# Kernel tuning notes

Hardware: AMD Instinct MI355X
Metric: run time of the kernel (lower is better)

## Reference

```python
import jax, jax.numpy as jnp
import numpy as np

EPS = 1e-8
SCALE_FACTOR = 5.0
ITERS = 3

def _ln(x, g, b):
    m = x.mean(-1, keepdims=True)
    v = ((x - m) ** 2).mean(-1, keepdims=True)
    return (x - m) / jnp.sqrt(v + 1e-5) * g + b

def setup_inputs() -> dict:
    key = jax.random.key(0)
    ks = jax.random.split(key, 12)
    B, N, K, D = 8, 1024, 8, 256
    n01 = lambda k, s, sc=0.02: jax.random.normal(k, s, jnp.float32) * sc
    return {
        "inputs": jax.random.normal(ks[0], (B, N, D), jnp.float32),
        "conditioning": jax.random.normal(ks[1], (B, K, D + 4), jnp.float32),
        "ni_g": jnp.ones((D,), jnp.float32), "ni_b": jnp.zeros((D,), jnp.float32),
        "ns_g": jnp.ones((D,), jnp.float32), "ns_b": jnp.zeros((D,), jnp.float32),
        "wq": n01(ks[2], (D, D)), "wk": n01(ks[3], (D, D)), "wv": n01(ks[4], (D, D)),
        "gp_w": n01(ks[5], (2, D), 0.5), "gp_b": jnp.zeros((D,), jnp.float32),
        "ge_ln_g": jnp.ones((D,), jnp.float32), "ge_ln_b": jnp.zeros((D,), jnp.float32),
        "ge_w1": n01(ks[6], (D, 2 * D)), "ge_b1": jnp.zeros((2 * D,), jnp.float32),
        "ge_w2": n01(ks[7], (2 * D, D)), "ge_b2": jnp.zeros((D,), jnp.float32),
        "gru_wih": n01(ks[8], (3 * D, D)), "gru_whh": n01(ks[9], (3 * D, D)),
        "gru_bih": jnp.zeros((3 * D,), jnp.float32), "gru_bhh": jnp.zeros((3 * D,), jnp.float32),
    }

def _forward(inputs, conditioning, ni_g, ni_b, ns_g, ns_b, wq, wk, wv,
             gp_w, gp_b, ge_ln_g, ge_ln_b, ge_w1, ge_b1, ge_w2, ge_b2,
             gru_wih, gru_whh, gru_bih, gru_bhh):
    B, N, FD = inputs.shape
    D = wq.shape[1]
    attn_scale = D ** -0.5
    side = int(round(N ** 0.5))
    xs = jnp.linspace(-1.0, 1.0, side)
    abs_grid = jnp.stack(jnp.meshgrid(xs, xs, indexing="ij"), -1).reshape(N, 2)  # (N,2)

    x = _ln(inputs, ni_g, ni_b)
    k = x @ wk  # (B,N,D)
    v = x @ wv  # (B,N,D)

    def grid_enc(t):
        h = _ln(t, ge_ln_g, ge_ln_b)
        h = jax.nn.relu(h @ ge_w1 + ge_b1)
        return h @ ge_w2 + ge_b2

    def step(slots_full, update):
        slots = slots_full[..., :-4]                       # (B,K,D)
        pos = jnp.clip(slots_full[..., -4:-2], -1.0, 1.0)  # (B,K,2)
        scl = jnp.clip(slots_full[..., -2:], 1e-3, 2.0)    # (B,K,2)
        rel_grid = (abs_grid[None, None] - pos[:, :, None]) / (scl[:, :, None] * SCALE_FACTOR)  # (B,K,N,2)
        rel_enc = rel_grid @ gp_w + gp_b                   # (B,K,N,D)
        rel_k = grid_enc(k[:, None] + rel_enc)             # (B,K,N,D)
        rel_v = grid_enc(v[:, None] + rel_enc)             # (B,K,N,D)
        q = _ln(slots, ns_g, ns_b) @ wq                    # (B,K,D)
        dots = jnp.einsum("bkd,bknd->bkn", q, rel_k) * attn_scale
        attn0 = jax.nn.softmax(dots, axis=1)               # softmax over the SLOT axis
        attn = attn0 + EPS
        attn = attn / attn.sum(-1, keepdims=True)
        pos_n = jnp.einsum("bkn,nd->bkd", attn0, abs_grid)
        spread = (abs_grid[None, None] - pos_n[:, :, None]) ** 2  # (B,K,N,2)
        scl_n = jnp.clip(jnp.sqrt(jnp.einsum("bkn,bknd->bkd", attn0 + EPS, spread)), 1e-3, 2.0)
        if update:
            upd = jnp.einsum("bknd,bkn->bkd", rel_v, attn)
            gx = upd @ gru_wih.T + gru_bih
            gh = slots @ gru_whh.T + gru_bhh
            xr, xz, xn = jnp.split(gx, 3, -1)
            hr, hz, hn = jnp.split(gh, 3, -1)
            r = jax.nn.sigmoid(xr + hr)
            z = jax.nn.sigmoid(xz + hz)
            n_ = jnp.tanh(xn + r * hn)
            slots = (1.0 - z) * n_ + z * slots
        return jnp.concatenate([slots, pos_n, scl_n], -1), attn0, rel_grid

    attn0 = rel_grid = None
    for i in range(ITERS + 1):
        conditioning, attn0, rel_grid = step(conditioning, i < ITERS)
    return conditioning, attn0, rel_grid

def reference(inputs, conditioning, ni_g, ni_b, ns_g, ns_b, wq, wk, wv,
              gp_w, gp_b, ge_ln_g, ge_ln_b, ge_w1, ge_b1, ge_w2, ge_b2,
              gru_wih, gru_whh, gru_bih, gru_bhh):
    return _forward(inputs, conditioning, ni_g, ni_b, ns_g, ns_b, wq, wk, wv,
                    gp_w, gp_b, ge_ln_g, ge_ln_b, ge_w1, ge_b1, ge_w2, ge_b2,
                    gru_wih, gru_whh, gru_bih, gru_bhh)
```

## Files before the change

kernel.cpp:

```cpp
#include <hip/hip_runtime.h>
#include <math.h>

#define NB 8
#define NN 1024
#define NK 8
#define ND 256
#define ND2 512
#define NBK 64
#define EPSA 1e-8f
#define LNEPS 1e-5f
#define GSTEP (2.0f/31.0f)

using short8 = __attribute__((ext_vector_type(8))) short;
using short4v = __attribute__((ext_vector_type(4))) short;
using floatx4 = __attribute__((ext_vector_type(4))) float;

__device__ __forceinline__ short f2bf(float f) {
  unsigned u = __builtin_bit_cast(unsigned, f);
  u += 0x7fffu + ((u >> 16) & 1u);
  return (short)(u >> 16);
}
__device__ __forceinline__ float bf2f(short s) {
  unsigned u = ((unsigned)(unsigned short)s) << 16;
  return __builtin_bit_cast(float, u);
}

__global__ __launch_bounds__(256) void k_cvt_all(
    const float* __restrict__ w1, const float* __restrict__ w2,
    const float* __restrict__ wk, const float* __restrict__ wv,
    const float* __restrict__ wih, const float* __restrict__ whh,
    const float* __restrict__ wq, const float* __restrict__ b2,
    short* __restrict__ w1T, short* __restrict__ wkT, short* __restrict__ wvT,
    short* __restrict__ whhB, short* __restrict__ w2B,
    float* __restrict__ bx, float* __restrict__ vb) {
  const int idx = blockIdx.x * 256 + threadIdx.x;
  if (idx < 131072) {
    const int n = idx >> 8, k = idx & 255;
    const int dst = ((n >> 4) * 8 + (k >> 5)) * 512 + ((k >> 3) & 3) * 128 + (n & 15) * 8 + (k & 7);
    w1T[dst] = f2bf(w1[(size_t)k * 512 + n]);
  } else if (idx < 196608) {
    const int i = idx - 131072;
    const int n = i >> 8, k = i & 255;
    const int dst = ((n >> 4) * 8 + (k >> 5)) * 512 + ((k >> 3) & 3) * 128 + (n & 15) * 8 + (k & 7);
    wkT[dst] = f2bf(wk[(size_t)k * 256 + n]);
  } else if (idx < 262144) {
    const int i = idx - 196608;
    const int n = i >> 8, k = i & 255;
    const int dst = ((n >> 4) * 8 + (k >> 5)) * 512 + ((k >> 3) & 3) * 128 + (n & 15) * 8 + (k & 7);
    wvT[dst] = f2bf(wv[(size_t)k * 256 + n]);
  } else if (idx < 458752) {
    const int i = idx - 262144;
    whhB[i] = f2bf(whh[i]);
  } else if (idx < 589824) {
    const int i = idx - 458752;
    w2B[i] = f2bf(w2[i]);
  } else if (idx < 590592) {
    const int j = idx - 589824;
    float s = 0.f;
#pragma unroll 8
    for (int d = 0; d < 256; d++) s = fmaf(b2[d], wih[(size_t)j * 256 + d], s);
    bx[j] = s;
  } else if (idx < 590848) {
    const int e = idx - 590592;
    float s = 0.f;
#pragma unroll 8
    for (int d = 0; d < 256; d++) s = fmaf(wq[(size_t)e * 256 + d], b2[d], s);
    vb[e] = s;
  }
}

__global__ __launch_bounds__(256, 2) void k_mm(
    const float* __restrict__ wih, const float* __restrict__ wq,
    const short* __restrict__ w2B,
    short* __restrict__ WXT, short* __restrict__ MQ) {
  const int z = blockIdx.z;
  if (z == 1 && blockIdx.x >= 4) return;
  const float* __restrict__ A = z ? wq : wih;
  short* __restrict__ C = z ? MQ : WXT;
  __shared__ __align__(16) short As[64 * 264];
  const int row0 = blockIdx.x * 64;
  const int col0 = blockIdx.y * 128;
  const int t = threadIdx.x;
  const int wave = t >> 6, lane = t & 63, l15 = lane & 15, quad = lane >> 4;
  {
    const int r = t >> 2, sub = t & 3;
    const float* ar = A + (size_t)(row0 + r) * 256;
#pragma unroll
    for (int ii = 0; ii < 16; ii++) {
      const int d = sub * 4 + ii * 16;
      const float4 v = *(const float4*)(ar + d);
      short4v pk = {f2bf(v.x), f2bf(v.y), f2bf(v.z), f2bf(v.w)};
      *(short4v*)&As[r * 264 + d] = pk;
    }
  }
  __syncthreads();
  const short* wp = w2B + (size_t)(col0 + wave * 32 + l15) * 256 + quad * 8;
  floatx4 acc[4][2];
#pragma unroll
  for (int mt = 0; mt < 4; mt++)
#pragma unroll
    for (int nt = 0; nt < 2; nt++) acc[mt][nt] = (floatx4){0.f, 0.f, 0.f, 0.f};
#pragma unroll
  for (int kk = 0; kk < 8; kk++) {
    short8 af[4];
#pragma unroll
    for (int mt = 0; mt < 4; mt++)
      af[mt] = *(const short8*)&As[(mt * 16 + l15) * 264 + kk * 32 + quad * 8];
    short8 bf[2];
#pragma unroll
    for (int nt = 0; nt < 2; nt++)
      bf[nt] = *(const short8*)(wp + nt * 16 * 256 + kk * 32);
#pragma unroll
    for (int mt = 0; mt < 4; mt++)
#pragma unroll
      for (int nt = 0; nt < 2; nt++)
        acc[mt][nt] = __builtin_amdgcn_mfma_f32_16x16x32_bf16(af[mt], bf[nt], acc[mt][nt], 0, 0, 0);
  }
#pragma unroll
  for (int mt = 0; mt < 4; mt++)
#pragma unroll
    for (int nt = 0; nt < 2; nt++)
#pragma unroll
      for (int j = 0; j < 4; j++)
        C[(size_t)(row0 + mt * 16 + quad * 4 + j) * 512 + col0 + wave * 32 + nt * 16 + l15] =
            f2bf(acc[mt][nt][j]);
}

__global__ __launch_bounds__(256, 2) void k_gemm_kv_mfma(
    const float* __restrict__ inp,
    const float* __restrict__ nig, const float* __restrict__ nib,
    const short* __restrict__ wkT, const short* __restrict__ wvT,
    float* __restrict__ kout, float* __restrict__ vout) {
  __shared__ __align__(16) short tln[64 * 264];
  const short* __restrict__ WT = blockIdx.z ? wvT : wkT;
  float* __restrict__ out = blockIdx.z ? vout : kout;
  const int row0 = blockIdx.x * 64;
  const int t = threadIdx.x;
  const int wave = t >> 6, lane = t & 63, l15 = lane & 15, quad = lane >> 4;
  {
    const int r = t >> 2, sub = t & 3;
    const float* xr = inp + (size_t)(row0 + r) * ND;
    float tv[64];
    float sum = 0.f, ssq = 0.f;
#pragma unroll
    for (int ii = 0; ii < 16; ii++) {
      const int d = sub * 4 + ii * 16;
      const float4 xv = *(const float4*)(xr + d);
      tv[ii * 4 + 0] = xv.x; sum += xv.x; ssq += xv.x * xv.x;
      tv[ii * 4 + 1] = xv.y; sum += xv.y; ssq += xv.y * xv.y;
      tv[ii * 4 + 2] = xv.z; sum += xv.z; ssq += xv.z * xv.z;
      tv[ii * 4 + 3] = xv.w; sum += xv.w; ssq += xv.w * xv.w;
    }
    sum += __shfl_xor(sum, 1); ssq += __shfl_xor(ssq, 1);
    sum += __shfl_xor(sum, 2); ssq += __shfl_xor(ssq, 2);
    const float mean = sum * (1.0f / ND);
    const float var = ssq * (1.0f / ND) - mean * mean;
    const float rstd = rsqrtf(var + LNEPS);
#pragma unroll
    for (int ii = 0; ii < 16; ii++) {
      const int d = sub * 4 + ii * 16;
      const float4 gg = *(const float4*)(nig + d);
      const float4 bb = *(const float4*)(nib + d);
      short4v pk;
      pk.x = f2bf((tv[ii * 4 + 0] - mean) * rstd * gg.x + bb.x);
      pk.y = f2bf((tv[ii * 4 + 1] - mean) * rstd * gg.y + bb.y);
      pk.z = f2bf((tv[ii * 4 + 2] - mean) * rstd * gg.z + bb.z);
      pk.w = f2bf((tv[ii * 4 + 3] - mean) * rstd * gg.w + bb.w);
      *(short4v*)&tln[r * 264 + d] = pk;
    }
  }
  __syncthreads();
  floatx4 acc[4][4];
#pragma unroll
  for (int mt = 0; mt < 4; mt++)
#pragma unroll
    for (int nt = 0; nt < 4; nt++) acc[mt][nt] = (floatx4){0.f, 0.f, 0.f, 0.f};
  const short* wp = WT + (size_t)(wave * 32) * 512 + (size_t)lane * 8;
#pragma unroll
  for (int kk = 0; kk < 8; kk++) {
    short8 af[4];
#pragma unroll
    for (int mt = 0; mt < 4; mt++)
      af[mt] = *(const short8*)&tln[(mt * 16 + l15) * 264 + kk * 32 + quad * 8];
    short8 bf[4];
#pragma unroll
    for (int nt = 0; nt < 4; nt++)
      bf[nt] = *(const short8*)(wp + (nt * 8 + kk) * 512);
#pragma unroll
    for (int mt = 0; mt < 4; mt++)
#pragma unroll
      for (int nt = 0; nt < 4; nt++)
        acc[mt][nt] = __builtin_amdgcn_mfma_f32_16x16x32_bf16(af[mt], bf[nt], acc[mt][nt], 0, 0, 0);
  }
#pragma unroll
  for (int mt = 0; mt < 4; mt++)
#pragma unroll
    for (int nt = 0; nt < 4; nt++)
#pragma unroll
      for (int j = 0; j < 4; j++)
        out[(size_t)(row0 + mt * 16 + quad * 4 + j) * ND + wave * 64 + nt * 16 + l15] = acc[mt][nt][j];
}

#define LDA 264

__global__ __launch_bounds__(256, 2) void k_fused_mfma(
    const float* __restrict__ kv,
    const float* __restrict__ pos, const float* __restrict__ scl,
    const float* __restrict__ gpw, const float* __restrict__ gpb,
    const float* __restrict__ lng, const float* __restrict__ lnb,
    const short* __restrict__ w1T, const float* __restrict__ b1,
    const float* __restrict__ w2q, float* __restrict__ dots,
    const float* __restrict__ attn0, const float* __restrict__ stage,
    float* __restrict__ ph, const int mode) {
  __shared__ __align__(16) short tln[64 * LDA];

  const int bk = blockIdx.y;
  const int n0 = blockIdx.x * 64;
  const int b = bk >> 3;
  const int t = threadIdx.x;
  const int wave = t >> 6;
  const int lane = t & 63;
  const int l15 = lane & 15;
  const int quad = lane >> 4;

  {
    const float p0 = pos[bk * 2 + 0], p1 = pos[bk * 2 + 1];
    const float s0i = 1.0f / (scl[bk * 2 + 0] * 5.0f);
    const float s1i = 1.0f / (scl[bk * 2 + 1] * 5.0f);
    const int r = t >> 2;
    const int sub = t & 3;
    const int n = n0 + r;
    const float gx = -1.0f + GSTEP * (float)(n >> 5);
    const float gy = -1.0f + GSTEP * (float)(n & 31);
    const float rg0 = (gx - p0) * s0i;
    const float rg1 = (gy - p1) * s1i;
    const float* kvrow = kv + (size_t)(b * NN + n) * ND;
    float tv[64];
    float sum = 0.f, ssq = 0.f;
#pragma unroll
    for (int ii = 0; ii < 16; ii++) {
      const int d = sub * 4 + ii * 16;
      const float4 kv4 = *(const float4*)(kvrow + d);
      const float4 wa = *(const float4*)(gpw + d);
      const float4 wb = *(const float4*)(gpw + ND + d);
      const float4 pb = *(const float4*)(gpb + d);
      float v0 = kv4.x + rg0 * wa.x + rg1 * wb.x + pb.x;
      float v1 = kv4.y + rg0 * wa.y + rg1 * wb.y + pb.y;
      float v2 = kv4.z + rg0 * wa.z + rg1 * wb.z + pb.z;
      float v3 = kv4.w + rg0 * wa.w + rg1 * wb.w + pb.w;
      tv[ii * 4 + 0] = v0; sum += v0; ssq += v0 * v0;
      tv[ii * 4 + 1] = v1; sum += v1; ssq += v1 * v1;
      tv[ii * 4 + 2] = v2; sum += v2; ssq += v2 * v2;
      tv[ii * 4 + 3] = v3; sum += v3; ssq += v3 * v3;
    }
    sum += __shfl_xor(sum, 1); ssq += __shfl_xor(ssq, 1);
    sum += __shfl_xor(sum, 2); ssq += __shfl_xor(ssq, 2);
    const float mean = sum * (1.0f / ND);
    const float var = ssq * (1.0f / ND) - mean * mean;
    const float rstd = rsqrtf(var + LNEPS);
#pragma unroll
    for (int ii = 0; ii < 16; ii++) {
      const int d = sub * 4 + ii * 16;
      const float4 gg = *(const float4*)(lng + d);
      const float4 bb = *(const float4*)(lnb + d);
      short4v pk;
      pk.x = f2bf((tv[ii * 4 + 0] - mean) * rstd * gg.x + bb.x);
      pk.y = f2bf((tv[ii * 4 + 1] - mean) * rstd * gg.y + bb.y);
      pk.z = f2bf((tv[ii * 4 + 2] - mean) * rstd * gg.z + bb.z);
      pk.w = f2bf((tv[ii * 4 + 3] - mean) * rstd * gg.w + bb.w);
      *(short4v*)&tln[r * LDA + d] = pk;
    }
  }
  __syncthreads();

  floatx4 acc1[4][8];
#pragma unroll
  for (int mt = 0; mt < 4; mt++)
#pragma unroll
    for (int nt = 0; nt < 8; nt++) acc1[mt][nt] = (floatx4){0.f, 0.f, 0.f, 0.f};

  const short* w1p = w1T + (size_t)(wave * 64) * 512 + (size_t)lane * 8;
#pragma unroll
  for (int kk = 0; kk < 8; kk++) {
    short8 af[4];
#pragma unroll
    for (int mt = 0; mt < 4; mt++)
      af[mt] = *(const short8*)&tln[(mt * 16 + l15) * LDA + kk * 32 + quad * 8];
    short8 bf[8];
#pragma unroll
    for (int nt = 0; nt < 8; nt++)
      bf[nt] = *(const short8*)(w1p + (nt * 8 + kk) * 512);
#pragma unroll
    for (int mt = 0; mt < 4; mt++)
#pragma unroll
      for (int nt = 0; nt < 8; nt++)
        acc1[mt][nt] = __builtin_amdgcn_mfma_f32_16x16x32_bf16(af[mt], bf[nt], acc1[mt][nt], 0, 0, 0);
  }

  float b1v[8];
#pragma unroll
  for (int nt = 0; nt < 8; nt++) b1v[nt] = b1[wave * 128 + nt * 16 + l15];

  if (mode == 0) {
    float w2qv[8];
#pragma unroll
    for (int nt = 0; nt < 8; nt++) w2qv[nt] = w2q[bk * 512 + wave * 128 + nt * 16 + l15];
    const float qb2 = stage[bk * 8 + 5];
    __syncthreads();
    float* dred = (float*)tln;
#pragma unroll
    for (int mt = 0; mt < 4; mt++)
#pragma unroll
      for (int j = 0; j < 4; j++) {
        float p = 0.f;
#pragma unroll
        for (int nt = 0; nt < 8; nt++)
          p = fmaf(fmaxf(acc1[mt][nt][j] + b1v[nt], 0.f), w2qv[nt], p);
        p += __shfl_xor(p, 1); p += __shfl_xor(p, 2);
        p += __shfl_xor(p, 4); p += __shfl_xor(p, 8);
        if (l15 == 0) dred[wave * 64 + mt * 16 + quad * 4 + j] = p;
      }
    __syncthreads();
    if (t < 64) {
      const float s = dred[t] + dred[64 + t] + dred[128 + t] + dred[192 + t];
      dots[bk * NN + n0 + t] = (s + qb2) * 0.0625f;
    }
  } else {
    const float dn = 1.0f / (stage[bk * 8 + 0] + (float)NN * EPSA);
    float aw[4][4];
#pragma unroll
    for (int mt = 0; mt < 4; mt++)
#pragma unroll
      for (int j = 0; j < 4; j++)
        aw[mt][j] = (attn0[bk * NN + n0 + mt * 16 + quad * 4 + j] + EPSA) * dn;
#pragma unroll
    for (int nt = 0; nt < 8; nt++) {
      float cs = 0.f;
#pragma unroll
      for (int mt = 0; mt < 4; mt++)
#pragma unroll
        for (int j = 0; j < 4; j++)
          cs = fmaf(aw[mt][j], fmaxf(acc1[mt][nt][j] + b1v[nt], 0.f), cs);
      cs += __shfl_xor(cs, 16); cs += __shfl_xor(cs, 32);
      if (quad == 0) atomicAdd(ph + bk * 512 + wave * 128 + nt * 16 + l15, cs);
    }
  }
}

__global__ __launch_bounds__(256) void k_softmax_reduce(
    const float* __restrict__ dots, float* __restrict__ attn0,
    float* __restrict__ stage) {
  const int t = threadIdx.x;
  const int idx = blockIdx.x * 256 + t;
  const int b = idx >> 10, n = idx & 1023;
  const int lane = t & 63, wave = t >> 6;
  float vals[NK];
  float mx = -1e30f;
#pragma unroll
  for (int k = 0; k < NK; k++) {
    vals[k] = dots[(size_t)(b * NK + k) * NN + n];
    mx = fmaxf(mx, vals[k]);
  }
  float s = 0.f;
#pragma unroll
  for (int k = 0; k < NK; k++) { vals[k] = expf(vals[k] - mx); s += vals[k]; }
  const float inv = 1.0f / s;
  const float gx = -1.0f + GSTEP * (float)(n >> 5);
  const float gy = -1.0f + GSTEP * (float)(n & 31);
  const float gx2 = gx * gx, gy2 = gy * gy;
  float sk[NK][5];
#pragma unroll
  for (int k = 0; k < NK; k++) {
    const float a = vals[k] * inv;
    attn0[(size_t)(b * NK + k) * NN + n] = a;
    const float w = a + EPSA;
    sk[k][0] = a;
    sk[k][1] = a * gx;
    sk[k][2] = a * gy;
    sk[k][3] = w * gx2;
    sk[k][4] = w * gy2;
  }
#pragma unroll
  for (int m = 32; m >= 1; m >>= 1)
#pragma unroll
    for (int k = 0; k < NK; k++)
#pragma unroll
      for (int c = 0; c < 5; c++)
        sk[k][c] += __shfl_xor(sk[k][c], m);
  __shared__ float red[4][40];
  if (lane == 0) {
#pragma unroll
    for (int k = 0; k < NK; k++)
#pragma unroll
      for (int c = 0; c < 5; c++)
        red[wave][k * 5 + c] = sk[k][c];
  }
  __syncthreads();
  if (t < 40) {
    const float tot = red[0][t] + red[1][t] + red[2][t] + red[3][t];
    const int k = t / 5, c = t % 5;
    atomicAdd(&stage[(b * NK + k) * 8 + c], tot);
  }
}

__global__ __launch_bounds__(256) void k_gatesC(
    const float* __restrict__ ph, const float* __restrict__ sf,
    const short* __restrict__ WXT, const short* __restrict__ whhB,
    const float* __restrict__ bx, short* __restrict__ gxh) {
  __shared__ __align__(16) short A[64 * 264];
  const int c = blockIdx.x;
  const int isX = (c < 6) ? 1 : 0;
  const int jb = (isX ? c : c - 6) * 128;
  const int t = threadIdx.x;
  const int wave = t >> 6, lane = t & 63, l15 = lane & 15, quad = lane >> 4;
  const int r = t >> 2, sub = t & 3;
  floatx4 acc[4][2];
#pragma unroll
  for (int mt = 0; mt < 4; mt++)
#pragma unroll
    for (int nt = 0; nt < 2; nt++) acc[mt][nt] = (floatx4){0.f, 0.f, 0.f, 0.f};

  if (isX) {
#pragma unroll
    for (int half = 0; half < 2; half++) {
      if (half > 0) __syncthreads();
#pragma unroll
      for (int ii = 0; ii < 16; ii++) {
        const int d = sub * 4 + ii * 16;
        const float4 v = *(const float4*)(ph + r * 512 + half * 256 + d);
        short4v pk = {f2bf(v.x), f2bf(v.y), f2bf(v.z), f2bf(v.w)};
        *(short4v*)&A[r * 264 + d] = pk;
      }
      __syncthreads();
      const short* wp = WXT + (size_t)(jb + wave * 32 + l15) * 512 + half * 256 + quad * 8;
#pragma unroll
      for (int kk = 0; kk < 8; kk++) {
        short8 af[4];
#pragma unroll
        for (int mt = 0; mt < 4; mt++)
          af[mt] = *(const short8*)&A[(mt * 16 + l15) * 264 + kk * 32 + quad * 8];
        short8 bf[2];
#pragma unroll
        for (int nt = 0; nt < 2; nt++)
          bf[nt] = *(const short8*)(wp + nt * 16 * 512 + kk * 32);
#pragma unroll
        for (int mt = 0; mt < 4; mt++)
#pragma unroll
          for (int nt = 0; nt < 2; nt++)
            acc[mt][nt] = __builtin_amdgcn_mfma_f32_16x16x32_bf16(af[mt], bf[nt], acc[mt][nt], 0, 0, 0);
      }
    }
#pragma unroll
    for (int nt = 0; nt < 2; nt++) {
      const int col = jb + wave * 32 + nt * 16 + l15;
      const float bxv = bx[col];
#pragma unroll
      for (int mt = 0; mt < 4; mt++)
#pragma unroll
        for (int j = 0; j < 4; j++)
          gxh[(mt * 16 + quad * 4 + j) * 1536 + col] = f2bf(acc[mt][nt][j] + bxv);
    }
  } else {
#pragma unroll
    for (int ii = 0; ii < 16; ii++) {
      const int d = sub * 4 + ii * 16;
      const float4 v = *(const float4*)(sf + r * 260 + d);
      short4v pk = {f2bf(v.x), f2bf(v.y), f2bf(v.z), f2bf(v.w)};
      *(short4v*)&A[r * 264 + d] = pk;
    }
    __syncthreads();
    const short* wp = whhB + (size_t)(jb + wave * 32 + l15) * 256 + quad * 8;
#pragma unroll
    for (int kk = 0; kk < 8; kk++) {
      short8 af[4];
#pragma unroll
      for (int mt = 0; mt < 4; mt++)
        af[mt] = *(const short8*)&A[(mt * 16 + l15) * 264 + kk * 32 + quad * 8];
      short8 bf[2];
#pragma unroll
      for (int nt = 0; nt < 2; nt++)
        bf[nt] = *(const short8*)(wp + nt * 16 * 256 + kk * 32);
#pragma unroll
      for (int mt = 0; mt < 4; mt++)
#pragma unroll
        for (int nt = 0; nt < 2; nt++)
          acc[mt][nt] = __builtin_amdgcn_mfma_f32_16x16x32_bf16(af[mt], bf[nt], acc[mt][nt], 0, 0, 0);
    }
#pragma unroll
    for (int mt = 0; mt < 4; mt++)
#pragma unroll
      for (int nt = 0; nt < 2; nt++)
#pragma unroll
        for (int j = 0; j < 4; j++)
          gxh[(mt * 16 + quad * 4 + j) * 1536 + 768 + jb + wave * 32 + nt * 16 + l15] =
              f2bf(acc[mt][nt][j]);
    }
}

__global__ __launch_bounds__(256) void k_slotW(
    const short* __restrict__ gxh, float* __restrict__ sf,
    const float* __restrict__ cond,
    const float* __restrict__ bih, const float* __restrict__ bhh,
    const float* __restrict__ nsg, const float* __restrict__ nsb,
    const short* __restrict__ MQ, const float* __restrict__ vb,
    float* __restrict__ w2q, float* __restrict__ pos, float* __restrict__ scl,
    float* __restrict__ stage, float* __restrict__ ph, const int mode) {
  const int bk = blockIdx.x, t = threadIdx.x;
  __shared__ float lnvS[256];
  __shared__ float red[8];
  const int wv = t >> 6;
  float ns;
  if (mode) {
    const float h = sf[bk * 260 + t];
    const float x0 = bf2f(gxh[bk * 1536 + t]);
    const float x1 = bf2f(gxh[bk * 1536 + 256 + t]);
    const float x2 = bf2f(gxh[bk * 1536 + 512 + t]);
    const float h0 = bf2f(gxh[bk * 1536 + 768 + t]);
    const float h1v = bf2f(gxh[bk * 1536 + 1024 + t]);
    const float h2 = bf2f(gxh[bk * 1536 + 1280 + t]);
    const float r = 1.0f / (1.0f + expf(-(x0 + bih[t] + h0 + bhh[t])));
    const float z = 1.0f / (1.0f + expf(-(x1 + bih[256 + t] + h1v + bhh[256 + t])));
    const float nw = tanhf(x2 + bih[512 + t] + r * (h2 + bhh[512 + t]));
    ns = (1.0f - z) * nw + z * h;
    sf[bk * 260 + t] = ns;
  } else {
    ns = cond[bk * 260 + t];
    sf[bk * 260 + t] = ns;
    if (t < 4) sf[bk * 260 + 256 + t] = cond[bk * 260 + 256 + t];
  }
  float s2 = ns, ss = ns * ns;
#pragma unroll
  for (int m = 32; m >= 1; m >>= 1) { s2 += __shfl_xor(s2, m); ss += __shfl_xor(ss, m); }
  if ((t & 63) == 0) { red[wv] = s2; red[4 + wv] = ss; }
  __syncthreads();
  const float S = red[0] + red[1] + red[2] + red[3];
  const float SS = red[4] + red[5] + red[6] + red[7];
  const float mean = S * (1.0f / ND);
  const float var = SS * (1.0f / ND) - mean * mean;
  const float rstd = rsqrtf(var + LNEPS);
  const float lnv = (ns - mean) * rstd * nsg[t] + nsb[t];
  lnvS[t] = lnv;
  if (mode) {
    if (t == 0) {
      const float Sa = stage[bk * 8 + 0];
      const float G0 = stage[bk * 8 + 1];
      const float G1 = stage[bk * 8 + 2];
      const float Q0 = stage[bk * 8 + 3];
      const float Q1 = stage[bk * 8 + 4];
      const float W = Sa + (float)NN * EPSA;
      const float sc0 = sqrtf(fmaxf(Q0 - 2.0f * G0 * G0 + G0 * G0 * W, 0.f));
      const float sc1 = sqrtf(fmaxf(Q1 - 2.0f * G1 * G1 + G1 * G1 * W, 0.f));
      const float sc0c = fminf(fmaxf(sc0, 1e-3f), 2.0f);
      const float sc1c = fminf(fmaxf(sc1, 1e-3f), 2.0f);
      sf[bk * 260 + 256] = G0;
      sf[bk * 260 + 257] = G1;
      sf[bk * 260 + 258] = sc0c;
      sf[bk * 260 + 259] = sc1c;
      pos[bk * 2 + 0] = fminf(fmaxf(G0, -1.0f), 1.0f);
      pos[bk * 2 + 1] = fminf(fmaxf(G1, -1.0f), 1.0f);
      scl[bk * 2 + 0] = sc0c;
      scl[bk * 2 + 1] = sc1c;
    }
  } else {
    if (t < 2) {
      const float p = cond[bk * 260 + 256 + t];
      pos[bk * 2 + t] = fminf(fmaxf(p, -1.0f), 1.0f);
      const float sc = cond[bk * 260 + 258 + t];
      scl[bk * 2 + t] = fminf(fmaxf(sc, 1e-3f), 2.0f);
    }
  }
  __syncthreads();
  if (t < 5) stage[bk * 8 + t] = 0.f;
  ph[bk * 512 + t] = 0.f;
  ph[bk * 512 + 256 + t] = 0.f;
  float w0 = 0.f, w1v = 0.f;
#pragma unroll 8
  for (int e = 0; e < ND; e++) {
    const float lv = lnvS[e];
    w0 = fmaf(lv, bf2f(MQ[e * 512 + t]), w0);
    w1v = fmaf(lv, bf2f(MQ[e * 512 + 256 + t]), w1v);
  }
  w2q[bk * 512 + t] = w0;
  w2q[bk * 512 + 256 + t] = w1v;
  float qd = lnvS[t] * vb[t];
#pragma unroll
  for (int m = 32; m >= 1; m >>= 1) qd += __shfl_xor(qd, m);
  __syncthreads();
  if ((t & 63) == 0) red[wv] = qd;
  __syncthreads();
  if (t == 0) stage[bk * 8 + 5] = red[0] + red[1] + red[2] + red[3];
}

__global__ __launch_bounds__(256) void k_finalize(
    const float* __restrict__ sf, const float* __restrict__ attn0,
    const float* __restrict__ pos, const float* __restrict__ scl,
    const float* __restrict__ stage, float* __restrict__ out) {
  const int bk = blockIdx.x, t = threadIdx.x;
  out[bk * 260 + t] = sf[bk * 260 + t];
  if (t == 0) {
    const float Sa = stage[bk * 8 + 0];
    const float G0 = stage[bk * 8 + 1];
    const float G1 = stage[bk * 8 + 2];
    const float Q0 = stage[bk * 8 + 3];
    const float Q1 = stage[bk * 8 + 4];
    const float W = Sa + (float)NN * EPSA;
    const float sc0 = sqrtf(fmaxf(Q0 - 2.0f * G0 * G0 + G0 * G0 * W, 0.f));
    const float sc1 = sqrtf(fmaxf(Q1 - 2.0f * G1 * G1 + G1 * G1 * W, 0.f));
    out[bk * 260 + 256] = G0;
    out[bk * 260 + 257] = G1;
    out[bk * 260 + 258] = fminf(fmaxf(sc0, 1e-3f), 2.0f);
    out[bk * 260 + 259] = fminf(fmaxf(sc1, 1e-3f), 2.0f);
  }
  const float p0 = pos[bk * 2 + 0], p1 = pos[bk * 2 + 1];
  const float s0 = scl[bk * 2 + 0] * 5.0f, s1 = scl[bk * 2 + 1] * 5.0f;
#pragma unroll
  for (int i = 0; i < 4; i++) {
    const int n = t + 256 * i;
    out[16640 + bk * NN + n] = attn0[(size_t)bk * NN + n];
    const float gx = -1.0f + GSTEP * (float)(n >> 5);
    const float gy = -1.0f + GSTEP * (float)(n & 31);
    float2 v;
    v.x = (gx - p0) / s0;
    v.y = (gy - p1) / s1;
    *(float2*)(out + 16640 + 65536 + ((size_t)bk * NN + n) * 2) = v;
  }
}

extern "C" void kernel_launch(void* const* d_in, const int* in_sizes, int n_in,
                              void* d_out, int out_size, void* d_ws, size_t ws_size,
                              hipStream_t stream) {
  const float* inputs   = (const float*)d_in[0];
  const float* cond     = (const float*)d_in[1];
  const float* ni_g     = (const float*)d_in[2];
  const float* ni_b     = (const float*)d_in[3];
  const float* ns_g     = (const float*)d_in[4];
  const float* ns_b     = (const float*)d_in[5];
  const float* wq       = (const float*)d_in[6];
  const float* wk       = (const float*)d_in[7];
  const float* wv       = (const float*)d_in[8];
  const float* gp_w     = (const float*)d_in[9];
  const float* gp_b     = (const float*)d_in[10];
  const float* ge_ln_g  = (const float*)d_in[11];
  const float* ge_ln_b  = (const float*)d_in[12];
  const float* ge_w1    = (const float*)d_in[13];
  const float* ge_b1    = (const float*)d_in[14];
  const float* ge_w2    = (const float*)d_in[15];
  const float* ge_b2    = (const float*)d_in[16];
  const float* gru_wih  = (const float*)d_in[17];
  const float* gru_whh  = (const float*)d_in[18];
  const float* gru_bih  = (const float*)d_in[19];
  const float* gru_bhh  = (const float*)d_in[20];

  float* ws   = (float*)d_ws;
  float* kbuf = ws;
  float* vbuf = kbuf + 2097152;
  float* sf   = vbuf + 2097152;
  float* w2qb = sf + 16640;
  float* posb = w2qb + 32768;
  float* sclb = posb + 128;
  float* dotsb = sclb + 128;
  float* at0  = dotsb + 65536;
  float* phb  = at0 + 65536;
  float* stag = phb + 32768;
  float* bxb  = stag + 512;
  float* vbb  = bxb + 768;
  short* gxh  = (short*)(vbb + 256);
  short* w1T  = gxh + 98304;
  short* wkT  = w1T + 131072;
  short* wvT  = wkT + 65536;
  short* whhB = wvT + 65536;
  short* w2B  = whhB + 196608;
  short* WXT  = w2B + 131072;
  short* MQ   = WXT + 393216;

  float* out = (float*)d_out;

  k_cvt_all<<<2308, 256, 0, stream>>>(ge_w1, ge_w2, wk, wv, gru_wih, gru_whh, wq,
                                      ge_b2, w1T, wkT, wvT, whhB, w2B, bxb, vbb);
  k_mm<<<dim3(12, 4, 2), 256, 0, stream>>>(gru_wih, wq, w2B, WXT, MQ);
  k_gemm_kv_mfma<<<dim3(128, 1, 2), 256, 0, stream>>>(inputs, ni_g, ni_b,
                                                      wkT, wvT, kbuf, vbuf);
  k_slotW<<<NBK, 256, 0, stream>>>(gxh, sf, cond, gru_bih, gru_bhh, ns_g, ns_b,
                                   MQ, vbb, w2qb, posb, sclb, stag, phb, 0);

  for (int s = 0; s < 4; s++) {
    k_fused_mfma<<<dim3(16, NBK), 256, 0, stream>>>(
        kbuf, posb, sclb, gp_w, gp_b, ge_ln_g, ge_ln_b, w1T, ge_b1,
        w2qb, dotsb, at0, stag, phb, 0);
    k_softmax_reduce<<<32, 256, 0, stream>>>(dotsb, at0, stag);
    if (s < 3) {
      k_fused_mfma<<<dim3(16, NBK), 256, 0, stream>>>(
          vbuf, posb, sclb, gp_w, gp_b, ge_ln_g, ge_ln_b, w1T, ge_b1,
          w2qb, dotsb, at0, stag, phb, 1);
      k_gatesC<<<12, 256, 0, stream>>>(phb, sf, WXT, whhB, bxb, gxh);
      k_slotW<<<NBK, 256, 0, stream>>>(gxh, sf, cond, gru_bih, gru_bhh, ns_g, ns_b,
                                       MQ, vbb, w2qb, posb, sclb, stag, phb, 1);
    }
  }

  k_finalize<<<NBK, 256, 0, stream>>>(sf, at0, posb, sclb, stag, out);
}
```

Baseline: 447.3 us.

## Hoist slot-independent grid-encoder GEMM out of iterations via LayerNorm decomposition

The grid-encoder input is k (or v) plus a rank-2 positional term, so its LayerNorm moments and the first linear layer are expanded algebraically. The slot-independent part (x+gp_b)*g @ W1 is computed once per k and v with MFMA and stored as bf16. Each iteration then rebuilds the pre-activation from that, a few rank-1 correction vectors and per-row moments, removing the 64 GEMMs per slot per iteration. The attention-weighted reduction now writes per-block partials to a buffer that a separate kernel sums, replacing the atomics. The cost is a larger workspace, more memory traffic reading the bf16 KW rows for every slot, and numerics that now depend on the moment-based variance formula.

```diff
diff --git a/kernel.cpp b/kernel.cpp
--- a/kernel.cpp
+++ b/kernel.cpp
@@ -201,150 +201,284 @@
         out[(size_t)(row0 + mt * 16 + quad * 4 + j) * ND + wave * 64 + nt * 16 + l15] = acc[mt][nt][j];
 }
 
-#define LDA 264
-
-__global__ __launch_bounds__(256, 2) void k_fused_mfma(
-    const float* __restrict__ kv,
+__global__ __launch_bounds__(256, 2) void k_kw(
+    const float* __restrict__ kbuf, const float* __restrict__ vbuf,
+    const float* __restrict__ gpb, const float* __restrict__ gpw,
+    const float* __restrict__ lng,
+    const short* __restrict__ w1T,
+    short* __restrict__ KWk, short* __restrict__ KWv,
+    float* __restrict__ momk, float* __restrict__ momv) {
+  __shared__ __align__(16) short tln[64 * 264];
+  const float* __restrict__ src = blockIdx.z ? vbuf : kbuf;
+  short* __restrict__ KW = blockIdx.z ? KWv : KWk;
+  float* __restrict__ mom = blockIdx.z ? momv : momk;
+  const int row0 = blockIdx.x * 64;
+  const int t = threadIdx.x;
+  const int wave = t >> 6, lane = t & 63, l15 = lane & 15, quad = lane >> 4;
+  {
+    const int r = t >> 2, sub = t & 3;
+    const float* xr = src + (size_t)(row0 + r) * ND;
+    float su = 0.f, sq = 0.f, sa = 0.f, sb = 0.f;
+#pragma unroll
+    for (int ii = 0; ii < 16; ii++) {
+      const int d = sub * 4 + ii * 16;
+      const float4 xv = *(const float4*)(xr + d);
+      const float4 pb = *(const float4*)(gpb + d);
+      const float4 wa = *(const float4*)(gpw + d);
+      const float4 wb = *(const float4*)(gpw + ND + d);
+      const float4 gg = *(const float4*)(lng + d);
+      const float u0 = xv.x + pb.x, u1 = xv.y + pb.y, u2 = xv.z + pb.z, u3 = xv.w + pb.w;
+      su += u0 + u1 + u2 + u3;
+      sq += u0 * u0 + u1 * u1 + u2 * u2 + u3 * u3;
+      sa += u0 * wa.x + u1 * wa.y + u2 * wa.z + u3 * wa.w;
+      sb += u0 * wb.x + u1 * wb.y + u2 * wb.z + u3 * wb.w;
+      short4v pk = {f2bf(u0 * gg.x), f2bf(u1 * gg.y), f2bf(u2 * gg.z), f2bf(u3 * gg.w)};
+      *(short4v*)&tln[r * 264 + d] = pk;
+    }
+    su += __shfl_xor(su, 1); sq += __shfl_xor(sq, 1);
+    sa += __shfl_xor(sa, 1); sb += __shfl_xor(sb, 1);
+    su += __shfl_xor(su, 2); sq += __shfl_xor(sq, 2);
+    sa += __shfl_xor(sa, 2); sb += __shfl_xor(sb, 2);
+    if (sub == 0) {
+      mom[(size_t)(row0 + r) * 4 + 0] = su * (1.0f / ND);
+      mom[(size_t)(row0 + r) * 4 + 1] = sq * (1.0f / ND);
+      mom[(size_t)(row0 + r) * 4 + 2] = sa * (1.0f / ND);
+      mom[(size_t)(row0 + r) * 4 + 3] = sb * (1.0f / ND);
+    }
+  }
+  __syncthreads();
+  floatx4 acc[4][8];
+#pragma unroll
+  for (int mt = 0; mt < 4; mt++)
+#pragma unroll
+    for (int nt = 0; nt < 8; nt++) acc[mt][nt] = (floatx4){0.f, 0.f, 0.f, 0.f};
+  const short* w1p = w1T + (size_t)(wave * 64) * 512 + (size_t)lane * 8;
+#pragma unroll
+  for (int kk = 0; kk < 8; kk++) {
+    short8 af[4];
+#pragma unroll
+    for (int mt = 0; mt < 4; mt++)
+      af[mt] = *(const short8*)&tln[(mt * 16 + l15) * 264 + kk * 32 + quad * 8];
+    short8 bf[8];
+#pragma unroll
+    for (int nt = 0; nt < 8; nt++)
+      bf[nt] = *(const short8*)(w1p + (nt * 8 + kk) * 512);
+#pragma unroll
+    for (int mt = 0; mt < 4; mt++)
+#pragma unroll
+      for (int nt = 0; nt < 8; nt++)
+        acc[mt][nt] = __builtin_amdgcn_mfma_f32_16x16x32_bf16(af[mt], bf[nt], acc[mt][nt], 0, 0, 0);
+  }
+#pragma unroll
+  for (int mt = 0; mt < 4; mt++)
+#pragma unroll
+    for (int nt = 0; nt < 8; nt++)
+#pragma unroll
+      for (int j = 0; j < 4; j++)
+        KW[(size_t)(row0 + mt * 16 + quad * 4 + j) * 512 + wave * 128 + nt * 16 + l15] =
+            f2bf(acc[mt][nt][j]);
+}
+
+__global__ __launch_bounds__(64) void k_vec(
+    const float* __restrict__ gpw, const float* __restrict__ lng,
+    const float* __restrict__ lnb, const float* __restrict__ w1,
+    const float* __restrict__ b1, float* __restrict__ vecs) {
+  const int v = blockIdx.x >> 3;
+  const int j = (blockIdx.x & 7) * 64 + threadIdx.x;
+  float s = 0.f;
+#pragma unroll 4
+  for (int d = 0; d < 256; d++) {
+    float c;
+    if (v == 0) c = gpw[d] * lng[d];
+    else if (v == 1) c = gpw[256 + d] * lng[d];
+    else if (v == 2) c = lng[d];
+    else c = lnb[d];
+    s = fmaf(c, w1[(size_t)d * 512 + j], s);
+  }
+  if (v == 3) s += b1[j];
+  vecs[v * 512 + j] = s;
+}
+
+__global__ __launch_bounds__(256) void k_scal(const float* __restrict__ gpw,
+                                              float* __restrict__ vecs) {
+  const int t = threadIdx.x;
+  const float wa = gpw[t], wb = gpw[256 + t];
+  float v0 = wa, v1 = wb, v2 = wa * wa, v3 = wb * wb, v4 = wa * wb;
+#pragma unroll
+  for (int m = 32; m >= 1; m >>= 1) {
+    v0 += __shfl_xor(v0, m); v1 += __shfl_xor(v1, m); v2 += __shfl_xor(v2, m);
+    v3 += __shfl_xor(v3, m); v4 += __shfl_xor(v4, m);
+  }
+  __shared__ float red[4][5];
+  if ((t & 63) == 0) {
+    red[t >> 6][0] = v0; red[t >> 6][1] = v1; red[t >> 6][2] = v2;
+    red[t >> 6][3] = v3; red[t >> 6][4] = v4;
+  }
+  __syncthreads();
+  if (t < 5)
+    vecs[2048 + t] = (red[0][t] + red[1][t] + red[2][t] + red[3][t]) * (1.0f / 256.0f);
+}
+
+__global__ __launch_bounds__(256) void k_dots(
+    const short* __restrict__ KW, const float* __restrict__ mom,
+    const float* __restrict__ vecs,
     const float* __restrict__ pos, const float* __restrict__ scl,
-    const float* __restrict__ gpw, const float* __restrict__ gpb,
-    const float* __restrict__ lng, const float* __restrict__ lnb,
-    const short* __restrict__ w1T, const float* __restrict__ b1,
-    const float* __restrict__ w2q, float* __restrict__ dots,
-    const float* __restrict__ attn0, const float* __restrict__ stage,
-    float* __restrict__ ph, const int mode) {
-  __shared__ __align__(16) short tln[64 * LDA];
-
-  const int bk = blockIdx.y;
-  const int n0 = blockIdx.x * 64;
-  const int b = bk >> 3;
-  const int t = threadIdx.x;
-  const int wave = t >> 6;
-  const int lane = t & 63;
-  const int l15 = lane & 15;
-  const int quad = lane >> 4;
-
-  {
-    const float p0 = pos[bk * 2 + 0], p1 = pos[bk * 2 + 1];
-    const float s0i = 1.0f / (scl[bk * 2 + 0] * 5.0f);
-    const float s1i = 1.0f / (scl[bk * 2 + 1] * 5.0f);
-    const int r = t >> 2;
-    const int sub = t & 3;
-    const int n = n0 + r;
+    const float* __restrict__ w2q, const float* __restrict__ stage,
+    float* __restrict__ dots) {
+  const int b = blockIdx.y, nt = blockIdx.x;
+  const int t = threadIdx.x, wave = t >> 6, lane = t & 63;
+  float AWv[8], BWv[8], GWv[8], bWv[8];
+#pragma unroll
+  for (int e = 0; e < 8; e++) {
+    const int j = e * 64 + lane;
+    AWv[e] = vecs[j]; BWv[e] = vecs[512 + j];
+    GWv[e] = vecs[1024 + j]; bWv[e] = vecs[1536 + j];
+  }
+  const float mwa = vecs[2048], mwb = vecs[2049];
+  const float ewa2 = vecs[2050], ewb2 = vecs[2051], ewab = vecs[2052];
+  float p0[8], p1[8], si0[8], si1[8], qb2[8];
+#pragma unroll
+  for (int k = 0; k < 8; k++) {
+    const int bk = b * 8 + k;
+    p0[k] = pos[bk * 2]; p1[k] = pos[bk * 2 + 1];
+    si0[k] = 1.0f / (scl[bk * 2] * 5.0f);
+    si1[k] = 1.0f / (scl[bk * 2 + 1] * 5.0f);
+    qb2[k] = stage[bk * 8 + 5];
+  }
+#pragma unroll
+  for (int i = 0; i < 2; i++) {
+    const int n = nt * 8 + wave * 2 + i;
+    const int row = b * NN + n;
+    float KWr[8];
+#pragma unroll
+    for (int e = 0; e < 8; e++) KWr[e] = bf2f(KW[(size_t)row * 512 + e * 64 + lane]);
+    const float mu = mom[row * 4 + 0], qm = mom[row * 4 + 1];
+    const float ca = mom[row * 4 + 2], cb = mom[row * 4 + 3];
     const float gx = -1.0f + GSTEP * (float)(n >> 5);
     const float gy = -1.0f + GSTEP * (float)(n & 31);
-    const float rg0 = (gx - p0) * s0i;
-    const float rg1 = (gy - p1) * s1i;
-    const float* kvrow = kv + (size_t)(b * NN + n) * ND;
-    float tv[64];
-    float sum = 0.f, ssq = 0.f;
-#pragma unroll
-    for (int ii = 0; ii < 16; ii++) {
-      const int d = sub * 4 + ii * 16;
-      const float4 kv4 = *(const float4*)(kvrow + d);
-      const float4 wa = *(const float4*)(gpw + d);
-      const float4 wb = *(const float4*)(gpw + ND + d);
-      const float4 pb = *(const float4*)(gpb + d);
-      float v0 = kv4.x + rg0 * wa.x + rg1 * wb.x + pb.x;
-      float v1 = kv4.y + rg0 * wa.y + rg1 * wb.y + pb.y;
-      float v2 = kv4.z + rg0 * wa.z + rg1 * wb.z + pb.z;
-      float v3 = kv4.w + rg0 * wa.w + rg1 * wb.w + pb.w;
-      tv[ii * 4 + 0] = v0; sum += v0; ssq += v0 * v0;
-      tv[ii * 4 + 1] = v1; sum += v1; ssq += v1 * v1;
-      tv[ii * 4 + 2] = v2; sum += v2; ssq += v2 * v2;
-      tv[ii * 4 + 3] = v3; sum += v3; ssq += v3 * v3;
-    }
-    sum += __shfl_xor(sum, 1); ssq += __shfl_xor(ssq, 1);
-    sum += __shfl_xor(sum, 2); ssq += __shfl_xor(ssq, 2);
-    const float mean = sum * (1.0f / ND);
-    const float var = ssq * (1.0f / ND) - mean * mean;
-    const float rstd = rsqrtf(var + LNEPS);
-#pragma unroll
-    for (int ii = 0; ii < 16; ii++) {
-      const int d = sub * 4 + ii * 16;
-      const float4 gg = *(const float4*)(lng + d);
-      const float4 bb = *(const float4*)(lnb + d);
-      short4v pk;
-      pk.x = f2bf((tv[ii * 4 + 0] - mean) * rstd * gg.x + bb.x);
-      pk.y = f2bf((tv[ii * 4 + 1] - mean) * rstd * gg.y + bb.y);
-      pk.z = f2bf((tv[ii * 4 + 2] - mean) * rstd * gg.z + bb.z);
-      pk.w = f2bf((tv[ii * 4 + 3] - mean) * rstd * gg.w + bb.w);
-      *(short4v*)&tln[r * LDA + d] = pk;
-    }
-  }
-  __syncthreads();
-
-  floatx4 acc1[4][8];
-#pragma unroll
-  for (int mt = 0; mt < 4; mt++)
-#pragma unroll
-    for (int nt = 0; nt < 8; nt++) acc1[mt][nt] = (floatx4){0.f, 0.f, 0.f, 0.f};
-
-  const short* w1p = w1T + (size_t)(wave * 64) * 512 + (size_t)lane * 8;
-#pragma unroll
-  for (int kk = 0; kk < 8; kk++) {
-    short8 af[4];
-#pragma unroll
-    for (int mt = 0; mt < 4; mt++)
-      af[mt] = *(const short8*)&tln[(mt * 16 + l15) * LDA + kk * 32 + quad * 8];
-    short8 bf[8];
-#pragma unroll
-    for (int nt = 0; nt < 8; nt++)
-      bf[nt] = *(const short8*)(w1p + (nt * 8 + kk) * 512);
-#pragma unroll
-    for (int mt = 0; mt < 4; mt++)
-#pragma unroll
-      for (int nt = 0; nt < 8; nt++)
-        acc1[mt][nt] = __builtin_amdgcn_mfma_f32_16x16x32_bf16(af[mt], bf[nt], acc1[mt][nt], 0, 0, 0);
-  }
-
-  float b1v[8];
-#pragma unroll
-  for (int nt = 0; nt < 8; nt++) b1v[nt] = b1[wave * 128 + nt * 16 + l15];
-
-  if (mode == 0) {
-    float w2qv[8];
-#pragma unroll
-    for (int nt = 0; nt < 8; nt++) w2qv[nt] = w2q[bk * 512 + wave * 128 + nt * 16 + l15];
-    const float qb2 = stage[bk * 8 + 5];
+#pragma unroll
+    for (int k = 0; k < 8; k++) {
+      const float rg0 = (gx - p0[k]) * si0[k];
+      const float rg1 = (gy - p1[k]) * si1[k];
+      const float mean = mu + rg0 * mwa + rg1 * mwb;
+      const float ey2 = qm + rg0 * rg0 * ewa2 + rg1 * rg1 * ewb2 +
+                        2.0f * (rg0 * ca + rg1 * cb + rg0 * rg1 * ewab);
+      const float rstd = rsqrtf(ey2 - mean * mean + LNEPS);
+      const float* wq = w2q + (size_t)(b * 8 + k) * 512;
+      float d = 0.f;
+#pragma unroll
+      for (int e = 0; e < 8; e++) {
+        float tt = KWr[e];
+        tt = fmaf(rg0, AWv[e], tt);
+        tt = fmaf(rg1, BWv[e], tt);
+        tt = fmaf(-mean, GWv[e], tt);
+        const float h = fmaf(rstd, tt, bWv[e]);
+        d = fmaf(fmaxf(h, 0.f), wq[e * 64 + lane], d);
+      }
+      d += __shfl_xor(d, 1); d += __shfl_xor(d, 2); d += __shfl_xor(d, 4);
+      d += __shfl_xor(d, 8); d += __shfl_xor(d, 16); d += __shfl_xor(d, 32);
+      if (lane == 0) dots[(size_t)(b * 8 + k) * NN + n] = (d + qb2[k]) * 0.0625f;
+    }
+  }
+}
+
+__global__ __launch_bounds__(256) void k_ph(
+    const short* __restrict__ KW, const float* __restrict__ mom,
+    const float* __restrict__ vecs,
+    const float* __restrict__ pos, const float* __restrict__ scl,
+    const float* __restrict__ attn0, const float* __restrict__ stage,
+    float* __restrict__ php) {
+  const int b = blockIdx.y, nt = blockIdx.x;
+  const int t = threadIdx.x, wave = t >> 6, lane = t & 63;
+  __shared__ float phs[8 * 512];
+  float AWv[8], BWv[8], GWv[8], bWv[8];
+#pragma unroll
+  for (int e = 0; e < 8; e++) {
+    const int j = e * 64 + lane;
+    AWv[e] = vecs[j]; BWv[e] = vecs[512 + j];
+    GWv[e] = vecs[1024 + j]; bWv[e] = vecs[1536 + j];
+  }
+  const float mwa = vecs[2048], mwb = vecs[2049];
+  const float ewa2 = vecs[2050], ewb2 = vecs[2051], ewab = vecs[2052];
+  float p0[8], p1[8], si0[8], si1[8], dn[8];
+#pragma unroll
+  for (int k = 0; k < 8; k++) {
+    const int bk = b * 8 + k;
+    p0[k] = pos[bk * 2]; p1[k] = pos[bk * 2 + 1];
+    si0[k] = 1.0f / (scl[bk * 2] * 5.0f);
+    si1[k] = 1.0f / (scl[bk * 2 + 1] * 5.0f);
+    dn[k] = 1.0f / (stage[bk * 8 + 0] + (float)NN * EPSA);
+  }
+  float acc[8][8];
+#pragma unroll
+  for (int k = 0; k < 8; k++)
+#pragma unroll
+    for (int e = 0; e < 8; e++) acc[k][e] = 0.f;
+#pragma unroll
+  for (int i = 0; i < 4; i++) {
+    const int n = nt * 16 + wave * 4 + i;
+    const int row = b * NN + n;
+    float KWr[8];
+#pragma unroll
+    for (int e = 0; e < 8; e++) KWr[e] = bf2f(KW[(size_t)row * 512 + e * 64 + lane]);
+    const float mu = mom[row * 4 + 0], qm = mom[row * 4 + 1];
+    const float ca = mom[row * 4 + 2], cb = mom[row * 4 + 3];
+    const float gx = -1.0f + GSTEP * (float)(n >> 5);
+    const float gy = -1.0f + GSTEP * (float)(n & 31);
+#pragma unroll
+    for (int k = 0; k < 8; k++) {
+      const float rg0 = (gx - p0[k]) * si0[k];
+      const float rg1 = (gy - p1[k]) * si1[k];
+      const float mean = mu + rg0 * mwa + rg1 * mwb;
+      const float ey2 = qm + rg0 * rg0 * ewa2 + rg1 * rg1 * ewb2 +
+                        2.0f * (rg0 * ca + rg1 * cb + rg0 * rg1 * ewab);
+      const float rstd = rsqrtf(ey2 - mean * mean + LNEPS);
+      const float aw = (attn0[(size_t)(b * 8 + k) * NN + n] + EPSA) * dn[k];
+#pragma unroll
+      for (int e = 0; e < 8; e++) {
+        float tt = KWr[e];
+        tt = fmaf(rg0, AWv[e], tt);
+        tt = fmaf(rg1, BWv[e], tt);
+        tt = fmaf(-mean, GWv[e], tt);
+        const float h = fmaf(rstd, tt, bWv[e]);
+        acc[k][e] = fmaf(aw, fmaxf(h, 0.f), acc[k][e]);
+      }
+    }
+  }
+#pragma unroll
+  for (int w = 0; w < 4; w++) {
+    if (wave == w) {
+#pragma unroll
+      for (int k = 0; k < 8; k++)
+#pragma unroll
+        for (int e = 0; e < 8; e++) {
+          const int j = e * 64 + lane;
+          if (w == 0) phs[k * 512 + j] = acc[k][e];
+          else phs[k * 512 + j] += acc[k][e];
+        }
+    }
     __syncthreads();
-    float* dred = (float*)tln;
-#pragma unroll
-    for (int mt = 0; mt < 4; mt++)
-#pragma unroll
-      for (int j = 0; j < 4; j++) {
-        float p = 0.f;
-#pragma unroll
-        for (int nt = 0; nt < 8; nt++)
-          p = fmaf(fmaxf(acc1[mt][nt][j] + b1v[nt], 0.f), w2qv[nt], p);
-        p += __shfl_xor(p, 1); p += __shfl_xor(p, 2);
-        p += __shfl_xor(p, 4); p += __shfl_xor(p, 8);
-        if (l15 == 0) dred[wave * 64 + mt * 16 + quad * 4 + j] = p;
-      }
-    __syncthreads();
-    if (t < 64) {
-      const float s = dred[t] + dred[64 + t] + dred[128 + t] + dred[192 + t];
-      dots[bk * NN + n0 + t] = (s + qb2) * 0.0625f;
-    }
-  } else {
-    const float dn = 1.0f / (stage[bk * 8 + 0] + (float)NN * EPSA);
-    float aw[4][4];
-#pragma unroll
-    for (int mt = 0; mt < 4; mt++)
-#pragma unroll
-      for (int j = 0; j < 4; j++)
-        aw[mt][j] = (attn0[bk * NN + n0 + mt * 16 + quad * 4 + j] + EPSA) * dn;
-#pragma unroll
-    for (int nt = 0; nt < 8; nt++) {
-      float cs = 0.f;
-#pragma unroll
-      for (int mt = 0; mt < 4; mt++)
-#pragma unroll
-        for (int j = 0; j < 4; j++)
-          cs = fmaf(aw[mt][j], fmaxf(acc1[mt][nt][j] + b1v[nt], 0.f), cs);
-      cs += __shfl_xor(cs, 16); cs += __shfl_xor(cs, 32);
-      if (quad == 0) atomicAdd(ph + bk * 512 + wave * 128 + nt * 16 + l15, cs);
-    }
-  }
+  }
+  float* dst = php + (size_t)(nt * 8 + b) * 4096;
+  const int base = t * 16;
+#pragma unroll
+  for (int q = 0; q < 4; q++)
+    *(float4*)(dst + base + q * 4) = *(const float4*)(phs + base + q * 4);
+}
+
+__global__ __launch_bounds__(256) void k_phred(const float* __restrict__ php,
+                                               float* __restrict__ ph) {
+  const int bk = blockIdx.x, t = threadIdx.x;
+  const int b = bk >> 3, k = bk & 7;
+  float s0 = 0.f, s1 = 0.f;
+#pragma unroll 4
+  for (int p = 0; p < 64; p++) {
+    const float* src = php + (size_t)(p * 8 + b) * 4096 + k * 512;
+    s0 += src[t];
+    s1 += src[t + 256];
+  }
+  ph[bk * 512 + t] = s0;
+  ph[bk * 512 + 256 + t] = s1;
 }
 
 __global__ __launch_bounds__(256) void k_softmax_reduce(
@@ -504,7 +638,7 @@
     const float* __restrict__ nsg, const float* __restrict__ nsb,
     const short* __restrict__ MQ, const float* __restrict__ vb,
     float* __restrict__ w2q, float* __restrict__ pos, float* __restrict__ scl,
-    float* __restrict__ stage, float* __restrict__ ph, const int mode) {
+    float* __restrict__ stage, const int mode) {
   const int bk = blockIdx.x, t = threadIdx.x;
   __shared__ float lnvS[256];
   __shared__ float red[8];
@@ -571,8 +705,6 @@
   }
   __syncthreads();
   if (t < 5) stage[bk * 8 + t] = 0.f;
-  ph[bk * 512 + t] = 0.f;
-  ph[bk * 512 + 256 + t] = 0.f;
   float w0 = 0.f, w1v = 0.f;
 #pragma unroll 8
   for (int e = 0; e < ND; e++) {
@@ -664,7 +796,11 @@
   float* stag = phb + 32768;
   float* bxb  = stag + 512;
   float* vbb  = bxb + 768;
-  short* gxh  = (short*)(vbb + 256);
+  float* momk = vbb + 256;
+  float* momv = momk + 32768;
+  float* vecs = momv + 32768;
+  float* php  = vecs + 2560;
+  short* gxh  = (short*)(php + 2097152);
   short* w1T  = gxh + 98304;
   short* wkT  = w1T + 131072;
   short* wvT  = wkT + 65536;
@@ -672,6 +808,8 @@
   short* w2B  = whhB + 196608;
   short* WXT  = w2B + 131072;
   short* MQ   = WXT + 393216;
+  short* KWk  = MQ + 131072;
+  short* KWv  = KWk + 4194304;
 
   float* out = (float*)d_out;
 
@@ -680,21 +818,24 @@
   k_mm<<<dim3(12, 4, 2), 256, 0, stream>>>(gru_wih, wq, w2B, WXT, MQ);
   k_gemm_kv_mfma<<<dim3(128, 1, 2), 256, 0, stream>>>(inputs, ni_g, ni_b,
                                                       wkT, wvT, kbuf, vbuf);
+  k_vec<<<32, 64, 0, stream>>>(gp_w, ge_ln_g, ge_ln_b, ge_w1, ge_b1, vecs);
+  k_scal<<<1, 256, 0, stream>>>(gp_w, vecs);
+  k_kw<<<dim3(128, 1, 2), 256, 0, stream>>>(kbuf, vbuf, gp_b, gp_w, ge_ln_g,
+                                            w1T, KWk, KWv, momk, momv);
   k_slotW<<<NBK, 256, 0, stream>>>(gxh, sf, cond, gru_bih, gru_bhh, ns_g, ns_b,
-                                   MQ, vbb, w2qb, posb, sclb, stag, phb, 0);
+                                   MQ, vbb, w2qb, posb, sclb, stag, 0);
 
   for (int s = 0; s < 4; s++) {
-    k_fused_mfma<<<dim3(16, NBK), 256, 0, stream>>>(
-        kbuf, posb, sclb, gp_w, gp_b, ge_ln_g, ge_ln_b, w1T, ge_b1,
-        w2qb, dotsb, at0, stag, phb, 0);
+    k_dots<<<dim3(128, NB), 256, 0, stream>>>(KWk, momk, vecs, posb, sclb,
+                                              w2qb, stag, dotsb);
     k_softmax_reduce<<<32, 256, 0, stream>>>(dotsb, at0, stag);
     if (s < 3) {
-      k_fused_mfma<<<dim3(16, NBK), 256, 0, stream>>>(
-          vbuf, posb, sclb, gp_w, gp_b, ge_ln_g, ge_ln_b, w1T, ge_b1,
-          w2qb, dotsb, at0, stag, phb, 1);
+      k_ph<<<dim3(64, NB), 256, 0, stream>>>(KWv, momv, vecs, posb, sclb,
+                                             at0, stag, php);
+      k_phred<<<NBK, 256, 0, stream>>>(php, phb);
       k_gatesC<<<12, 256, 0, stream>>>(phb, sf, WXT, whhB, bxb, gxh);
       k_slotW<<<NBK, 256, 0, stream>>>(gxh, sf, cond, gru_bih, gru_bhh, ns_g, ns_b,
-                                       MQ, vbb, w2qb, posb, sclb, stag, phb, 1);
+                                       MQ, vbb, w2qb, posb, sclb, stag, 1);
     }
   }
 
```

After: 484.0 us. 1.08x slower.
